# Kernel tuning notes

Measured on AMD Instinct MI355X. Metric: run time of the kernel, lower is better.

## Reference

```python
import jax, jax.numpy as jnp
import numpy as np
from jax import lax

B, D_MODEL, T = 4, 256, 8192
D_STATE, D_CONV = 16, 4
D_INNER = 2 * D_MODEL          # expand=2.0
DT_RANK = (D_MODEL + 15) // 16 # ceil(d_model/16) = 16
EPS = 1e-5


def setup_inputs() -> dict:
    key = jax.random.key(0)
    ks = jax.random.split(key, 12)
    s = lambda k, shape, scale=0.02: (jax.random.normal(k, shape, jnp.float32) * scale)
    x = jax.random.normal(ks[0], (B, D_MODEL, T), jnp.float32)
    ln_w = jnp.ones((D_MODEL,), jnp.float32)
    ln_b = jnp.zeros((D_MODEL,), jnp.float32)
    in_proj_w = s(ks[1], (2 * D_INNER, D_MODEL))
    conv_w = s(ks[2], (D_INNER, 1, D_CONV), 0.1)
    conv_b = jnp.zeros((D_INNER,), jnp.float32)
    x_proj_w = s(ks[3], (DT_RANK + 2 * D_STATE, D_INNER))
    dt_proj_w = s(ks[4], (D_INNER, DT_RANK), 0.1)
    # bias init so softplus(dt_bias) ~ small positive dt, like mamba_ssm
    dt_proj_b = jnp.log(jnp.expm1(jax.random.uniform(ks[5], (D_INNER,), jnp.float32, 0.001, 0.1)))
    # S4D-real init: A_log = log(1..d_state) broadcast over d_inner
    A_log = jnp.log(jnp.tile(jnp.arange(1, D_STATE + 1, dtype=jnp.float32), (D_INNER, 1)))
    D = jnp.ones((D_INNER,), jnp.float32)
    out_proj_w = s(ks[6], (D_MODEL, D_INNER))
    return {"x": x, "ln_w": ln_w, "ln_b": ln_b, "in_proj_w": in_proj_w,
            "conv_w": conv_w, "conv_b": conv_b, "x_proj_w": x_proj_w,
            "dt_proj_w": dt_proj_w, "dt_proj_b": dt_proj_b, "A_log": A_log,
            "D": D, "out_proj_w": out_proj_w}


def _mamba_block(x, ln_w, ln_b, in_proj_w, conv_w, conv_b, x_proj_w,
                 dt_proj_w, dt_proj_b, A_log, D, out_proj_w):
    # x: (B, C, T)
    residual = x
    xt = jnp.transpose(x, (0, 2, 1))  # (B, T, C)
    # channel layernorm
    mu = jnp.mean(xt, axis=-1, keepdims=True)
    var = jnp.var(xt, axis=-1, keepdims=True)
    xn = (xt - mu) * lax.rsqrt(var + EPS) * ln_w + ln_b
    # in_proj -> x, z
    xz = jnp.einsum('btc,ec->bte', xn, in_proj_w)  # (B,T,2*d_inner)
    x_in, z = jnp.split(xz, 2, axis=-1)
    # causal depthwise conv over time
    xc = jnp.transpose(x_in, (0, 2, 1))  # (B, d_inner, T)
    xc = lax.conv_general_dilated(xc, conv_w, window_strides=(1,),
                                  padding=[(D_CONV - 1, 0)],
                                  dimension_numbers=('NCH', 'OIH', 'NCH'),
                                  feature_group_count=D_INNER)
    xc = xc + conv_b[None, :, None]
    u = jax.nn.silu(jnp.transpose(xc, (0, 2, 1)))  # (B,T,d_inner)
    # x_proj -> dt, B, C
    dbl = jnp.einsum('btd,ed->bte', u, x_proj_w)
    dt, Bm, Cm = jnp.split(dbl, [DT_RANK, DT_RANK + D_STATE], axis=-1)
    delta = jax.nn.softplus(jnp.einsum('btr,dr->btd', dt, dt_proj_w) + dt_proj_b)  # (B,T,d_inner)
    A = -jnp.exp(A_log)  # (d_inner, d_state)
    deltaA = jnp.exp(jnp.einsum('btd,dn->btdn', delta, A))          # (B,T,d,n)
    deltaBu = jnp.einsum('btd,btn->btdn', delta * u, Bm)            # (B,T,d,n)
    # selective scan over time
    def step(h, inp):
        dA_t, dBu_t, C_t = inp
        h = dA_t * h + dBu_t                       # (B,d,n)
        y = jnp.einsum('bdn,bn->bd', h, C_t)
        return h, y
    h0 = jnp.zeros((x.shape[0], D_INNER, D_STATE), x.dtype)
    _, ys = lax.scan(step, h0, (jnp.moveaxis(deltaA, 1, 0),
                                jnp.moveaxis(deltaBu, 1, 0),
                                jnp.moveaxis(Cm, 1, 0)))
    y = jnp.moveaxis(ys, 0, 1) + u * D             # (B,T,d_inner)
    y = y * jax.nn.silu(z)
    out = jnp.einsum('btd,cd->btc', y, out_proj_w)  # (B,T,C)
    return jnp.transpose(out, (0, 2, 1)) + residual


def reference(x, ln_w, ln_b, in_proj_w, conv_w, conv_b, x_proj_w,
              dt_proj_w, dt_proj_b, A_log, D, out_proj_w):
    return _mamba_block(x, ln_w, ln_b, in_proj_w, conv_w, conv_b, x_proj_w,
                        dt_proj_w, dt_proj_b, A_log, D, out_proj_w)
```

## Files before the change

kernel.cpp:

```cpp
#include <hip/hip_runtime.h>

typedef unsigned short u16;
typedef unsigned int u32;
typedef __bf16 bfx8 __attribute__((ext_vector_type(8)));
typedef float f32x4 __attribute__((ext_vector_type(4)));

#define Tn 8192
#define Bn 4
#define MTOT 32768
#define CH 128
#define TC 64

#define OFF_W     0ul
#define OFF_AL2   917504ul
#define OFF_XN    (1ul<<20)
#define OFF_XIN   (17ul<<20)
#define OFF_Z     (49ul<<20)
#define OFF_U     (81ul<<20)
#define OFF_DBLDT (113ul<<20)
#define OFF_BCF   (115ul<<20)
#define OFF_DELTA (119ul<<20)
#define OFF_P     (151ul<<20)
#define OFF_CC    (167ul<<20)

__device__ __forceinline__ float b2f(u16 h){ return __uint_as_float(((u32)h)<<16); }
__device__ __forceinline__ u16 f2b(float f){
  u32 u = __float_as_uint(f);
  return (u16)((u + 0x7FFFu + ((u>>16)&1u)) >> 16);
}
__device__ __forceinline__ float aexp2(float x){ float r; asm("v_exp_f32 %0, %1" : "=v"(r) : "v"(x)); return r; }
__device__ __forceinline__ float arcp (float x){ float r; asm("v_rcp_f32 %0, %1" : "=v"(r) : "v"(x)); return r; }
__device__ __forceinline__ float alog2(float x){ float r; asm("v_log_f32 %0, %1" : "=v"(r) : "v"(x)); return r; }
__device__ __forceinline__ float fsilu(float a){ return a*arcp(1.f + aexp2(-a*1.44269504f)); }
__device__ __forceinline__ float fsoftplus(float v){
  float r = 0.69314718f*alog2(1.f + aexp2(v*1.44269504f));
  return (v > 20.f) ? v : r;
}
typedef const __attribute__((address_space(1))) void* gp1_t;
typedef __attribute__((address_space(3))) void* lp3_t;
__device__ __forceinline__ void gload_lds16(const void* g, void* l){
  __builtin_amdgcn_global_load_lds((gp1_t)g, (lp3_t)l, 16, 0, 0);
}

__global__ void wconv_k(const float* __restrict__ inw, const float* __restrict__ xpw,
                        const float* __restrict__ dtw, const float* __restrict__ opw,
                        const float* __restrict__ alog, u16* __restrict__ W, float* __restrict__ aL2)
{
  int i = blockIdx.x*256 + threadIdx.x;
  if (i < 262144) { W[i] = f2b(inw[i]); return; }
  if (i < 294912) { int j = i - 262144; int r = j >> 9, k = j & 511;
    float v = (r < 16) ? xpw[r*512 + k] : ((r < 32) ? 0.f : xpw[(r-16)*512 + k]);
    W[i] = f2b(v); return; }
  if (i < 311296) { int j = i - 294912; int d = j >> 5, k = j & 31;
    W[i] = f2b((k < 16) ? dtw[d*16 + k] : 0.f); return; }
  if (i < 442368) { W[i] = f2b(opw[i - 311296]); return; }
  if (i < 450560) { int j = i - 442368; aL2[j] = -__expf(alog[j]) * 1.44269504088896f; return; }
}

__global__ __launch_bounds__(256)
void ln_k(const float* __restrict__ x, const float* __restrict__ lnw,
          const float* __restrict__ lnb, u16* __restrict__ xn)
{
  const int t0 = blockIdx.x*64, b = blockIdx.y;
  const int tid = threadIdx.x, cg = tid>>6, tl = tid&63;
  __shared__ float ps[4][64], pq[4][64], mu[64], rs[64];
  float s = 0.f, q = 0.f;
  for (int ci = 0; ci < 64; ci++){
    int c = ci*4 + cg;
    float v = x[((size_t)(b*256 + c))*Tn + t0 + tl];
    s += v; q += v*v;
  }
  ps[cg][tl] = s; pq[cg][tl] = q;
  __syncthreads();
  if (tid < 64){
    float S = ps[0][tid]+ps[1][tid]+ps[2][tid]+ps[3][tid];
    float Q = pq[0][tid]+pq[1][tid]+pq[2][tid]+pq[3][tid];
    float m = S*(1.f/256.f);
    float var = Q*(1.f/256.f) - m*m;
    mu[tid] = m; rs[tid] = rsqrtf(var + 1e-5f);
  }
  __syncthreads();
  const float w = lnw[tid&255], bb = lnb[tid&255];
  for (int t = 0; t < 64; t++){
    float v = x[((size_t)(b*256 + tid))*Tn + t0 + t];
    xn[((size_t)(b*Tn) + t0 + t)*256 + tid] = f2b((v - mu[t])*rs[t]*w + bb);
  }
}

template<int BN, int EPI>
__global__ __launch_bounds__(256)
void gemm_k(const u16* __restrict__ A, int lda,
            const u16* __restrict__ Bw, int ldb,
            u16* __restrict__ O, u16* __restrict__ O2, float* __restrict__ Of, int ldo,
            const float* __restrict__ bias, int K)
{
  constexpr int NFR = BN/32;
  __shared__ __align__(16) u16 sA[128*32];
  __shared__ __align__(16) u16 sB[BN*32];
  const int tid = threadIdx.x;
  const int m0 = blockIdx.x*128, n0 = blockIdx.y*BN;
  const int lane = tid & 63, wid = tid >> 6;
  const int wr = wid >> 1, wc = wid & 1;
  const int lr = lane & 15, g = lane >> 4;
  const f32x4 fz = {0.f,0.f,0.f,0.f};
  f32x4 acc[4][NFR];
  #pragma unroll
  for (int m=0;m<4;m++)
    #pragma unroll
    for (int n=0;n<NFR;n++) acc[m][n] = fz;
  const int nk = K >> 5;
  for (int kt = 0; kt < nk; ++kt){
    __syncthreads();
    #pragma unroll
    for (int i=0;i<2;i++){ int ci = i*256 + tid;
      gload_lds16(A + (size_t)(m0+(ci>>2))*lda + kt*32 + (ci&3)*8, sA + ci*8); }
    #pragma unroll
    for (int i=0;i<BN/64;i++){ int ci = i*256 + tid;
      gload_lds16(Bw + (size_t)(n0+(ci>>2))*ldb + kt*32 + (ci&3)*8, sB + ci*8); }
    __syncthreads();
    bfx8 af[4], bf[NFR];
    #pragma unroll
    for (int m=0;m<4;m++) af[m] = *(const bfx8*)(sA + (wr*64 + m*16 + lr)*32 + g*8);
    #pragma unroll
    for (int n=0;n<NFR;n++) bf[n] = *(const bfx8*)(sB + (wc*(BN/2) + n*16 + lr)*32 + g*8);
    #pragma unroll
    for (int m=0;m<4;m++)
      #pragma unroll
      for (int n=0;n<NFR;n++)
        acc[m][n] = __builtin_amdgcn_mfma_f32_16x16x32_bf16(af[m], bf[n], acc[m][n], 0, 0, 0);
  }
  #pragma unroll
  for (int m=0;m<4;m++)
    #pragma unroll
    for (int n=0;n<NFR;n++)
      #pragma unroll
      for (int r=0;r<4;r++){
        int row = m0 + wr*64 + m*16 + g*4 + r;
        int col = n0 + wc*(BN/2) + n*16 + lr;
        float v = acc[m][n][r];
        if (EPI == 0){
          O[(size_t)row*ldo + col] = f2b(v);
        } else if (EPI == 1){
          O[(size_t)row*ldo + col] = f2b(fsoftplus(v + bias[col]));
        } else if (EPI == 2){
          if (col < 512) O[(size_t)row*512 + col] = f2b(v);
          else           O2[(size_t)row*512 + (col-512)] = f2b(v);
        } else {
          if (col < 32) O[(size_t)row*32 + col] = f2b(v);
          else          Of[(size_t)row*32 + (col-32)] = v;
        }
      }
}

__global__ __launch_bounds__(256)
void conv_k(const u16* __restrict__ xin, const float* __restrict__ cw,
            const float* __restrict__ cb, u16* __restrict__ u)
{
  const int t0 = blockIdx.x*32, d0 = blockIdx.y*64, b = blockIdx.z;
  const int tid = threadIdx.x;
  __shared__ float sx[35][64];
  __shared__ float sw[4][64];
  { int d = tid>>2, j = tid&3; sw[j][d] = cw[(d0+d)*4 + j]; }
  for (int i=0;i<9;i++){ int f = i*256 + tid; if (f < 35*64){
      int r = f>>6, dd = f&63; int t = t0 - 3 + r;
      sx[r][dd] = (t >= 0) ? b2f(xin[((size_t)(b*Tn)+t)*512 + d0+dd]) : 0.f; } }
  __syncthreads();
  const float cbv = cb[d0 + (tid&63)];
  for (int oi=0; oi<8; oi++){
    int f = oi*256 + tid; int tr = f>>6, dd = f&63;
    float a = cbv;
    #pragma unroll
    for (int j=0;j<4;j++) a += sw[j][dd]*sx[tr+j][dd];
    u[((size_t)(b*Tn)+t0+tr)*512 + d0+dd] = f2b(fsilu(a));
  }
}

__global__ __launch_bounds__(256)
void scanA_k(const u16* __restrict__ delta, const u16* __restrict__ u,
             const float* __restrict__ bcf, const float* __restrict__ aL2,
             float* __restrict__ P, float* __restrict__ CC)
{
  const int ch = blockIdx.x, d = blockIdx.y*256 + threadIdx.x, b = blockIdx.z;
  const int t0 = ch*TC;
  float aL[16], h[16];
  #pragma unroll
  for (int i=0;i<4;i++) *(f32x4*)(aL+4*i) = *(const f32x4*)(aL2 + (size_t)d*16 + 4*i);
  #pragma unroll
  for (int n=0;n<16;n++) h[n] = 0.f;
  bool st = true;
  #pragma unroll
  for (int n=1;n<16;n++) st = st && (fabsf(aL[n] - (n+1)*aL[0]) <= 2e-4f*fabsf(aL[n]));
  const u16* dp = delta + (size_t)(b*Tn + t0)*512 + d;
  const u16* up = u     + (size_t)(b*Tn + t0)*512 + d;
  const float* bp = bcf + (size_t)(b*Tn + t0)*32;
  float sdlt = 0.f;
  const float aL0 = aL[0];
  if (st){
    for (int t=0;t<TC;t++){
      float dlt = b2f(dp[(size_t)t*512]);
      float uu  = b2f(up[(size_t)t*512]);
      float Bv[16];
      #pragma unroll
      for (int i=0;i<4;i++) *(f32x4*)(Bv+4*i) = *(const f32x4*)(bp + (size_t)t*32 + 4*i);
      float du = dlt*uu; sdlt += dlt;
      float r = aexp2(dlt*aL0);
      float r2 = r*r, e = r, f = r2;
      #pragma unroll
      for (int n=0;n<16;n+=2){
        h[n]   = fmaf(e, h[n],   du*Bv[n]);
        h[n+1] = fmaf(f, h[n+1], du*Bv[n+1]);
        e *= r2; f *= r2;
      }
    }
  } else {
    for (int t=0;t<TC;t++){
      float dlt = b2f(dp[(size_t)t*512]);
      float uu  = b2f(up[(size_t)t*512]);
      float Bv[16];
      #pragma unroll
      for (int i=0;i<4;i++) *(f32x4*)(Bv+4*i) = *(const f32x4*)(bp + (size_t)t*32 + 4*i);
      float du = dlt*uu; sdlt += dlt;
      #pragma unroll
      for (int n=0;n<16;n++)
        h[n] = fmaf(aexp2(dlt*aL[n]), h[n], du*Bv[n]);
    }
  }
  float Pq[16];
  #pragma unroll
  for (int n=0;n<16;n++) Pq[n] = aexp2(sdlt*aL[n]);
  size_t o = ((size_t)((b*CH+ch)*512 + d))<<4;
  #pragma unroll
  for (int i=0;i<4;i++){
    *(f32x4*)(P +o+4*i) = *(f32x4*)(Pq+4*i);
    *(f32x4*)(CC+o+4*i) = *(f32x4*)(h +4*i);
  }
}

__global__ __launch_bounds__(256)
void scanB_k(float* __restrict__ P, const float* __restrict__ CC)
{
  const int gid = blockIdx.x*256 + threadIdx.x;
  const int b = gid >> 11, r = gid & 2047;
  const size_t base = (size_t)(r>>2)*16 + (size_t)(r&3)*4;
  f32x4 h = {0.f,0.f,0.f,0.f};
  #pragma unroll 4
  for (int ch=0; ch<CH; ch++){
    size_t idx = ((size_t)(b*CH+ch))*8192 + base;
    f32x4 Pv = *(f32x4*)(P+idx);
    f32x4 cv = *(const f32x4*)(CC+idx);
    *(f32x4*)(P+idx) = h;
    h = Pv*h + cv;
  }
}

__global__ __launch_bounds__(256)
void scanC_k(const u16* __restrict__ delta, const u16* __restrict__ u,
             const float* __restrict__ bcf, const u16* __restrict__ z,
             const float* __restrict__ aL2, const float* __restrict__ h0,
             const float* __restrict__ Dp, u16* __restrict__ yg)
{
  const int ch = blockIdx.x, d = blockIdx.y*256 + threadIdx.x, b = blockIdx.z;
  const int t0 = ch*TC;
  float aL[16], h[16];
  #pragma unroll
  for (int i=0;i<4;i++) *(f32x4*)(aL+4*i) = *(const f32x4*)(aL2 + (size_t)d*16 + 4*i);
  size_t o = ((size_t)((b*CH+ch)*512 + d))<<4;
  #pragma unroll
  for (int i=0;i<4;i++) *(f32x4*)(h+4*i) = *(const f32x4*)(h0+o+4*i);
  bool st = true;
  #pragma unroll
  for (int n=1;n<16;n++) st = st && (fabsf(aL[n] - (n+1)*aL[0]) <= 2e-4f*fabsf(aL[n]));
  const float Dd = Dp[d];
  const float aL0 = aL[0];
  const u16* dp = delta + (size_t)(b*Tn + t0)*512 + d;
  const u16* up = u     + (size_t)(b*Tn + t0)*512 + d;
  const u16* zp = z     + (size_t)(b*Tn + t0)*512 + d;
  const float* bp = bcf + (size_t)(b*Tn + t0)*32;
  u16* yp = yg + (size_t)(b*Tn + t0)*512 + d;
  if (st){
    for (int t=0;t<TC;t++){
      float dlt = b2f(dp[(size_t)t*512]);
      float uu  = b2f(up[(size_t)t*512]);
      float zz  = b2f(zp[(size_t)t*512]);
      float Bv[16], Cv[16];
      #pragma unroll
      for (int i=0;i<4;i++){
        *(f32x4*)(Bv+4*i) = *(const f32x4*)(bp + (size_t)t*32 + 4*i);
        *(f32x4*)(Cv+4*i) = *(const f32x4*)(bp + (size_t)t*32 + 16 + 4*i);
      }
      float du = dlt*uu;
      float r = aexp2(dlt*aL0);
      float r2 = r*r, e = r, f = r2;
      float p0=0.f, p1=0.f;
      #pragma unroll
      for (int n=0;n<16;n+=2){
        h[n]   = fmaf(e, h[n],   du*Bv[n]);   p0 = fmaf(h[n],   Cv[n],   p0);
        h[n+1] = fmaf(f, h[n+1], du*Bv[n+1]); p1 = fmaf(h[n+1], Cv[n+1], p1);
        e *= r2; f *= r2;
      }
      float p = p0 + p1;
      float gy = (p + uu*Dd) * fsilu(zz);
      yp[(size_t)t*512] = f2b(gy);
    }
  } else {
    for (int t=0;t<TC;t++){
      float dlt = b2f(dp[(size_t)t*512]);
      float uu  = b2f(up[(size_t)t*512]);
      float zz  = b2f(zp[(size_t)t*512]);
      float Bv[16], Cv[16];
      #pragma unroll
      for (int i=0;i<4;i++){
        *(f32x4*)(Bv+4*i) = *(const f32x4*)(bp + (size_t)t*32 + 4*i);
        *(f32x4*)(Cv+4*i) = *(const f32x4*)(bp + (size_t)t*32 + 16 + 4*i);
      }
      float du = dlt*uu;
      float p0 = 0.f;
      #pragma unroll
      for (int n=0;n<16;n++){
        h[n] = fmaf(aexp2(dlt*aL[n]), h[n], du*Bv[n]);
        p0 = fmaf(h[n], Cv[n], p0);
      }
      float gy = (p0 + uu*Dd) * fsilu(zz);
      yp[(size_t)t*512] = f2b(gy);
    }
  }
}

__global__ __launch_bounds__(256)
void transres_k(const u16* __restrict__ yt, const float* __restrict__ x, float* __restrict__ out)
{
  const int t0 = blockIdx.x*64, c0 = blockIdx.y*64, b = blockIdx.z;
  const int tid = threadIdx.x;
  __shared__ float st[64][65];
  for (int i=0;i<16;i++){ int f=i*256+tid; int tr=f>>6, cc=f&63;
    st[tr][cc] = b2f(yt[((size_t)(b*Tn)+t0+tr)*256 + c0+cc]); }
  __syncthreads();
  for (int i=0;i<16;i++){ int f=i*256+tid; int cr=f>>6, tt=f&63;
    size_t oa = ((size_t)(b*256)+c0+cr)*Tn + t0+tt;
    out[oa] = st[tt][cr] + x[oa]; }
}

extern "C" void kernel_launch(void* const* d_in, const int* in_sizes, int n_in,
                              void* d_out, int out_size, void* d_ws, size_t ws_size,
                              hipStream_t stream)
{
  const float* x    = (const float*)d_in[0];
  const float* lnw  = (const float*)d_in[1];
  const float* lnb  = (const float*)d_in[2];
  const float* inw  = (const float*)d_in[3];
  const float* cw   = (const float*)d_in[4];
  const float* cb   = (const float*)d_in[5];
  const float* xpw  = (const float*)d_in[6];
  const float* dtw  = (const float*)d_in[7];
  const float* dtb  = (const float*)d_in[8];
  const float* alog = (const float*)d_in[9];
  const float* Dp   = (const float*)d_in[10];
  const float* opw  = (const float*)d_in[11];
  float* out = (float*)d_out;
  char* ws = (char*)d_ws;

  u16*   W     = (u16*)(ws + OFF_W);
  float* aL2   = (float*)(ws + OFF_AL2);
  u16*   xn    = (u16*)(ws + OFF_XN);
  u16*   xin   = (u16*)(ws + OFF_XIN);
  u16*   z     = (u16*)(ws + OFF_Z);
  u16*   u     = (u16*)(ws + OFF_U);
  u16*   dblDT = (u16*)(ws + OFF_DBLDT);
  float* bcf   = (float*)(ws + OFF_BCF);
  u16*   delta = (u16*)(ws + OFF_DELTA);
  float* P     = (float*)(ws + OFF_P);
  float* CC    = (float*)(ws + OFF_CC);
  u16*   yg    = xin;
  u16*   ytmp  = xn;

  wconv_k<<<1760, 256, 0, stream>>>(inw, xpw, dtw, opw, alog, W, aL2);
  ln_k<<<dim3(Tn/64, Bn), 256, 0, stream>>>(x, lnw, lnb, xn);
  gemm_k<128,2><<<dim3(MTOT/128, 8), 256, 0, stream>>>(xn, 256, W, 256, xin, z, nullptr, 512, nullptr, 256);
  conv_k<<<dim3(Tn/32, 8, Bn), 256, 0, stream>>>(xin, cw, cb, u);
  gemm_k<64,3><<<dim3(MTOT/128, 1), 256, 0, stream>>>(u, 512, W + 262144, 512, dblDT, nullptr, bcf, 32, nullptr, 512);
  gemm_k<128,1><<<dim3(MTOT/128, 4), 256, 0, stream>>>(dblDT, 32, W + 294912, 32, delta, nullptr, nullptr, 512, dtb, 32);
  scanA_k<<<dim3(CH, 2, Bn), 256, 0, stream>>>(delta, u, bcf, aL2, P, CC);
  scanB_k<<<32, 256, 0, stream>>>(P, CC);
  scanC_k<<<dim3(CH, 2, Bn), 256, 0, stream>>>(delta, u, bcf, z, aL2, P, Dp, yg);
  gemm_k<128,0><<<dim3(MTOT/128, 2), 256, 0, stream>>>(yg, 512, W + 311296, 512, ytmp, nullptr, nullptr, 256, nullptr, 512);
  transres_k<<<dim3(Tn/64, 4, Bn), 256, 0, stream>>>(ytmp, x, out);
}
```

Measured before the change: 230.3 us.

## Fuse dt_proj+softplus into scan kernels and out_proj with transpose-residual

Removes the separate dt_proj GEMM and its bf16 delta buffer. Each scan kernel now recomputes delta per timestep from the 16-wide fp32 dt-rank projection, using a dot product with dt_proj weights followed by softplus. The output projection GEMM is fused with the transpose and residual add through an LDS staging tile, which drops the transres kernel and its intermediate buffer. The scan inner loops use packed fp32 FMA/mul instructions, and scanB is changed to scalar per-thread work across more blocks. The trade is extra ALU work in both scan passes in exchange for less memory traffic and fewer launches.

```diff
diff --git a/kernel.cpp b/kernel.cpp
--- a/kernel.cpp
+++ b/kernel.cpp
@@ -4,6 +4,7 @@
 typedef unsigned int u32;
 typedef __bf16 bfx8 __attribute__((ext_vector_type(8)));
 typedef float f32x4 __attribute__((ext_vector_type(4)));
+typedef float f32x2 __attribute__((ext_vector_type(2)));
 
 #define Tn 8192
 #define Bn 4
@@ -17,11 +18,10 @@
 #define OFF_XIN   (17ul<<20)
 #define OFF_Z     (49ul<<20)
 #define OFF_U     (81ul<<20)
-#define OFF_DBLDT (113ul<<20)
+#define OFF_DTF   (113ul<<20)
 #define OFF_BCF   (115ul<<20)
-#define OFF_DELTA (119ul<<20)
-#define OFF_P     (151ul<<20)
-#define OFF_CC    (167ul<<20)
+#define OFF_P     (119ul<<20)
+#define OFF_CC    (136ul<<20)
 
 __device__ __forceinline__ float b2f(u16 h){ return __uint_as_float(((u32)h)<<16); }
 __device__ __forceinline__ u16 f2b(float f){
@@ -36,6 +36,12 @@
   float r = 0.69314718f*alog2(1.f + aexp2(v*1.44269504f));
   return (v > 20.f) ? v : r;
 }
+__device__ __forceinline__ f32x2 pk_fma(f32x2 a, f32x2 b, f32x2 c){
+  f32x2 d; asm("v_pk_fma_f32 %0, %1, %2, %3" : "=v"(d) : "v"(a), "v"(b), "v"(c)); return d;
+}
+__device__ __forceinline__ f32x2 pk_mul(f32x2 a, f32x2 b){
+  f32x2 d; asm("v_pk_mul_f32 %0, %1, %2" : "=v"(d) : "v"(a), "v"(b)); return d;
+}
 typedef const __attribute__((address_space(1))) void* gp1_t;
 typedef __attribute__((address_space(3))) void* lp3_t;
 __device__ __forceinline__ void gload_lds16(const void* g, void* l){
@@ -43,7 +49,7 @@
 }
 
 __global__ void wconv_k(const float* __restrict__ inw, const float* __restrict__ xpw,
-                        const float* __restrict__ dtw, const float* __restrict__ opw,
+                        const float* __restrict__ opw,
                         const float* __restrict__ alog, u16* __restrict__ W, float* __restrict__ aL2)
 {
   int i = blockIdx.x*256 + threadIdx.x;
@@ -51,10 +57,8 @@
   if (i < 294912) { int j = i - 262144; int r = j >> 9, k = j & 511;
     float v = (r < 16) ? xpw[r*512 + k] : ((r < 32) ? 0.f : xpw[(r-16)*512 + k]);
     W[i] = f2b(v); return; }
-  if (i < 311296) { int j = i - 294912; int d = j >> 5, k = j & 31;
-    W[i] = f2b((k < 16) ? dtw[d*16 + k] : 0.f); return; }
-  if (i < 442368) { W[i] = f2b(opw[i - 311296]); return; }
-  if (i < 450560) { int j = i - 442368; aL2[j] = -__expf(alog[j]) * 1.44269504088896f; return; }
+  if (i < 425984) { W[i + 16384] = f2b(opw[i - 294912]); return; }
+  if (i < 434176) { int j = i - 425984; aL2[j] = -__expf(alog[j]) * 1.44269504088896f; return; }
 }
 
 __global__ __launch_bounds__(256)
@@ -91,8 +95,8 @@
 __global__ __launch_bounds__(256)
 void gemm_k(const u16* __restrict__ A, int lda,
             const u16* __restrict__ Bw, int ldb,
-            u16* __restrict__ O, u16* __restrict__ O2, float* __restrict__ Of, int ldo,
-            const float* __restrict__ bias, int K)
+            u16* __restrict__ O, u16* __restrict__ O2, float* __restrict__ Of,
+            float* __restrict__ Of2, int ldo, int K)
 {
   constexpr int NFR = BN/32;
   __shared__ __align__(16) u16 sA[128*32];
@@ -138,18 +142,76 @@
         int row = m0 + wr*64 + m*16 + g*4 + r;
         int col = n0 + wc*(BN/2) + n*16 + lr;
         float v = acc[m][n][r];
-        if (EPI == 0){
-          O[(size_t)row*ldo + col] = f2b(v);
-        } else if (EPI == 1){
-          O[(size_t)row*ldo + col] = f2b(fsoftplus(v + bias[col]));
-        } else if (EPI == 2){
+        if (EPI == 2){
           if (col < 512) O[(size_t)row*512 + col] = f2b(v);
           else           O2[(size_t)row*512 + (col-512)] = f2b(v);
         } else {
-          if (col < 32) O[(size_t)row*32 + col] = f2b(v);
-          else          Of[(size_t)row*32 + (col-32)] = v;
+          if (col < 16)       Of [(size_t)row*16 + col] = v;
+          else if (col >= 32) Of2[(size_t)row*32 + (col-32)] = v;
         }
       }
+}
+
+__global__ __launch_bounds__(256)
+void gemmot_k(const u16* __restrict__ A, const u16* __restrict__ Bw,
+              const float* __restrict__ x, float* __restrict__ out)
+{
+  __shared__ __align__(16) u16 sA[128*32];
+  __shared__ __align__(16) u16 sB[128*32];
+  __shared__ float st[64][129];
+  const int tid = threadIdx.x;
+  const int m0 = blockIdx.x*128, n0 = blockIdx.y*128;
+  const int lane = tid & 63, wid = tid >> 6;
+  const int wr = wid >> 1, wc = wid & 1;
+  const int lr = lane & 15, g = lane >> 4;
+  const f32x4 fz = {0.f,0.f,0.f,0.f};
+  f32x4 acc[4][4];
+  #pragma unroll
+  for (int m=0;m<4;m++)
+    #pragma unroll
+    for (int n=0;n<4;n++) acc[m][n] = fz;
+  for (int kt = 0; kt < 16; ++kt){
+    __syncthreads();
+    #pragma unroll
+    for (int i=0;i<2;i++){ int ci = i*256 + tid;
+      gload_lds16(A + (size_t)(m0+(ci>>2))*512 + kt*32 + (ci&3)*8, sA + ci*8); }
+    #pragma unroll
+    for (int i=0;i<2;i++){ int ci = i*256 + tid;
+      gload_lds16(Bw + (size_t)(n0+(ci>>2))*512 + kt*32 + (ci&3)*8, sB + ci*8); }
+    __syncthreads();
+    bfx8 af[4], bf[4];
+    #pragma unroll
+    for (int m=0;m<4;m++) af[m] = *(const bfx8*)(sA + (wr*64 + m*16 + lr)*32 + g*8);
+    #pragma unroll
+    for (int n=0;n<4;n++) bf[n] = *(const bfx8*)(sB + (wc*64 + n*16 + lr)*32 + g*8);
+    #pragma unroll
+    for (int m=0;m<4;m++)
+      #pragma unroll
+      for (int n=0;n<4;n++)
+        acc[m][n] = __builtin_amdgcn_mfma_f32_16x16x32_bf16(af[m], bf[n], acc[m][n], 0, 0, 0);
+  }
+  const int b = m0 >> 13, t0 = m0 & 8191;
+  const int tl = tid & 63, cgrp = tid >> 6;
+  for (int hf=0; hf<2; hf++){
+    __syncthreads();
+    if (wr == hf){
+      #pragma unroll
+      for (int m=0;m<4;m++)
+        #pragma unroll
+        for (int n=0;n<4;n++)
+          #pragma unroll
+          for (int r=0;r<4;r++)
+            st[m*16 + g*4 + r][wc*64 + n*16 + lr] = acc[m][n][r];
+    }
+    __syncthreads();
+    const int tg = t0 + hf*64 + tl;
+    #pragma unroll
+    for (int ci=0; ci<32; ci++){
+      int c = cgrp*32 + ci;
+      size_t oa = ((size_t)(b*256) + n0 + c)*Tn + tg;
+      out[oa] = st[tl][c] + x[oa];
+    }
+  }
 }
 
 __global__ __launch_bounds__(256)
@@ -176,49 +238,69 @@
 }
 
 __global__ __launch_bounds__(256)
-void scanA_k(const u16* __restrict__ delta, const u16* __restrict__ u,
-             const float* __restrict__ bcf, const float* __restrict__ aL2,
+void scanA_k(const float* __restrict__ dtf, const float* __restrict__ dtw, const float* __restrict__ dtb,
+             const u16* __restrict__ u, const float* __restrict__ bcf, const float* __restrict__ aL2,
              float* __restrict__ P, float* __restrict__ CC)
 {
   const int ch = blockIdx.x, d = blockIdx.y*256 + threadIdx.x, b = blockIdx.z;
   const int t0 = ch*TC;
-  float aL[16], h[16];
-  #pragma unroll
-  for (int i=0;i<4;i++) *(f32x4*)(aL+4*i) = *(const f32x4*)(aL2 + (size_t)d*16 + 4*i);
-  #pragma unroll
-  for (int n=0;n<16;n++) h[n] = 0.f;
+  float h[16], wv[16];
+  #pragma unroll
+  for (int i=0;i<4;i++) *(f32x4*)(wv+4*i) = *(const f32x4*)(dtw + (size_t)d*16 + 4*i);
+  #pragma unroll
+  for (int n=0;n<16;n++) h[n]=0.f;
+  const float dtbd = dtb[d];
+  const float aL0 = aL2[(size_t)d*16];
   bool st = true;
   #pragma unroll
-  for (int n=1;n<16;n++) st = st && (fabsf(aL[n] - (n+1)*aL[0]) <= 2e-4f*fabsf(aL[n]));
-  const u16* dp = delta + (size_t)(b*Tn + t0)*512 + d;
-  const u16* up = u     + (size_t)(b*Tn + t0)*512 + d;
+  for (int i=0;i<4;i++){
+    f32x4 av = *(const f32x4*)(aL2 + (size_t)d*16 + 4*i);
+    #pragma unroll
+    for (int k=0;k<4;k++){ int n = 4*i+k; st = st && (fabsf(av[k]-(n+1)*aL0) <= 2e-4f*fabsf(av[k])); }
+  }
+  const float* dtp = dtf + (size_t)(b*Tn + t0)*16;
+  const u16* up = u + (size_t)(b*Tn + t0)*512 + d;
   const float* bp = bcf + (size_t)(b*Tn + t0)*32;
   float sdlt = 0.f;
-  const float aL0 = aL[0];
   if (st){
     for (int t=0;t<TC;t++){
-      float dlt = b2f(dp[(size_t)t*512]);
-      float uu  = b2f(up[(size_t)t*512]);
-      float Bv[16];
+      float dr[16], Bv[16];
+      #pragma unroll
+      for (int i=0;i<4;i++) *(f32x4*)(dr+4*i) = *(const f32x4*)(dtp + (size_t)t*16 + 4*i);
       #pragma unroll
       for (int i=0;i<4;i++) *(f32x4*)(Bv+4*i) = *(const f32x4*)(bp + (size_t)t*32 + 4*i);
+      f32x2 a2 = {0.f,0.f};
+      #pragma unroll
+      for (int j=0;j<8;j++) a2 = pk_fma(*(f32x2*)(wv+2*j), *(f32x2*)(dr+2*j), a2);
+      float dlt = fsoftplus(a2.x + a2.y + dtbd);
+      float uu = b2f(up[(size_t)t*512]);
       float du = dlt*uu; sdlt += dlt;
       float r = aexp2(dlt*aL0);
-      float r2 = r*r, e = r, f = r2;
-      #pragma unroll
-      for (int n=0;n<16;n+=2){
-        h[n]   = fmaf(e, h[n],   du*Bv[n]);
-        h[n+1] = fmaf(f, h[n+1], du*Bv[n+1]);
-        e *= r2; f *= r2;
+      float r2 = r*r;
+      f32x2 ef = {r, r2}; const f32x2 rr = {r2, r2}; const f32x2 du2 = {du, du};
+      #pragma unroll
+      for (int j=0;j<8;j++){
+        f32x2 hb = *(f32x2*)(h+2*j);
+        hb = pk_fma(ef, hb, pk_mul(du2, *(f32x2*)(Bv+2*j)));
+        *(f32x2*)(h+2*j) = hb;
+        ef = pk_mul(ef, rr);
       }
     }
   } else {
+    float aL[16];
+    #pragma unroll
+    for (int i=0;i<4;i++) *(f32x4*)(aL+4*i) = *(const f32x4*)(aL2 + (size_t)d*16 + 4*i);
     for (int t=0;t<TC;t++){
-      float dlt = b2f(dp[(size_t)t*512]);
-      float uu  = b2f(up[(size_t)t*512]);
-      float Bv[16];
+      float dr[16], Bv[16];
+      #pragma unroll
+      for (int i=0;i<4;i++) *(f32x4*)(dr+4*i) = *(const f32x4*)(dtp + (size_t)t*16 + 4*i);
       #pragma unroll
       for (int i=0;i<4;i++) *(f32x4*)(Bv+4*i) = *(const f32x4*)(bp + (size_t)t*32 + 4*i);
+      float dot = dtbd;
+      #pragma unroll
+      for (int k=0;k<16;k++) dot = fmaf(wv[k], dr[k], dot);
+      float dlt = fsoftplus(dot);
+      float uu = b2f(up[(size_t)t*512]);
       float du = dlt*uu; sdlt += dlt;
       #pragma unroll
       for (int n=0;n<16;n++)
@@ -227,7 +309,11 @@
   }
   float Pq[16];
   #pragma unroll
-  for (int n=0;n<16;n++) Pq[n] = aexp2(sdlt*aL[n]);
+  for (int i=0;i<4;i++){
+    f32x4 av = *(const f32x4*)(aL2 + (size_t)d*16 + 4*i);
+    #pragma unroll
+    for (int k=0;k<4;k++) Pq[4*i+k] = aexp2(sdlt*av[k]);
+  }
   size_t o = ((size_t)((b*CH+ch)*512 + d))<<4;
   #pragma unroll
   for (int i=0;i<4;i++){
@@ -240,79 +326,100 @@
 void scanB_k(float* __restrict__ P, const float* __restrict__ CC)
 {
   const int gid = blockIdx.x*256 + threadIdx.x;
-  const int b = gid >> 11, r = gid & 2047;
-  const size_t base = (size_t)(r>>2)*16 + (size_t)(r&3)*4;
-  f32x4 h = {0.f,0.f,0.f,0.f};
+  const int b = gid >> 13, r = gid & 8191;
+  const size_t base = (size_t)b*CH*8192 + r;
+  float h = 0.f;
   #pragma unroll 4
   for (int ch=0; ch<CH; ch++){
-    size_t idx = ((size_t)(b*CH+ch))*8192 + base;
-    f32x4 Pv = *(f32x4*)(P+idx);
-    f32x4 cv = *(const f32x4*)(CC+idx);
-    *(f32x4*)(P+idx) = h;
-    h = Pv*h + cv;
-  }
-}
-
-__global__ __launch_bounds__(256)
-void scanC_k(const u16* __restrict__ delta, const u16* __restrict__ u,
-             const float* __restrict__ bcf, const u16* __restrict__ z,
+    size_t idx = base + (size_t)ch*8192;
+    float Pv = P[idx];
+    float cv = CC[idx];
+    P[idx] = h;
+    h = fmaf(Pv, h, cv);
+  }
+}
+
+__global__ __launch_bounds__(256)
+void scanC_k(const float* __restrict__ dtf, const float* __restrict__ dtw, const float* __restrict__ dtb,
+             const u16* __restrict__ u, const float* __restrict__ bcf, const u16* __restrict__ z,
              const float* __restrict__ aL2, const float* __restrict__ h0,
              const float* __restrict__ Dp, u16* __restrict__ yg)
 {
   const int ch = blockIdx.x, d = blockIdx.y*256 + threadIdx.x, b = blockIdx.z;
   const int t0 = ch*TC;
-  float aL[16], h[16];
-  #pragma unroll
-  for (int i=0;i<4;i++) *(f32x4*)(aL+4*i) = *(const f32x4*)(aL2 + (size_t)d*16 + 4*i);
+  float h[16], wv[16];
+  #pragma unroll
+  for (int i=0;i<4;i++) *(f32x4*)(wv+4*i) = *(const f32x4*)(dtw + (size_t)d*16 + 4*i);
   size_t o = ((size_t)((b*CH+ch)*512 + d))<<4;
   #pragma unroll
   for (int i=0;i<4;i++) *(f32x4*)(h+4*i) = *(const f32x4*)(h0+o+4*i);
+  const float dtbd = dtb[d];
+  const float Dd = Dp[d];
+  const float aL0 = aL2[(size_t)d*16];
   bool st = true;
   #pragma unroll
-  for (int n=1;n<16;n++) st = st && (fabsf(aL[n] - (n+1)*aL[0]) <= 2e-4f*fabsf(aL[n]));
-  const float Dd = Dp[d];
-  const float aL0 = aL[0];
-  const u16* dp = delta + (size_t)(b*Tn + t0)*512 + d;
-  const u16* up = u     + (size_t)(b*Tn + t0)*512 + d;
-  const u16* zp = z     + (size_t)(b*Tn + t0)*512 + d;
+  for (int i=0;i<4;i++){
+    f32x4 av = *(const f32x4*)(aL2 + (size_t)d*16 + 4*i);
+    #pragma unroll
+    for (int k=0;k<4;k++){ int n = 4*i+k; st = st && (fabsf(av[k]-(n+1)*aL0) <= 2e-4f*fabsf(av[k])); }
+  }
+  const float* dtp = dtf + (size_t)(b*Tn + t0)*16;
+  const u16* up = u + (size_t)(b*Tn + t0)*512 + d;
+  const u16* zp = z + (size_t)(b*Tn + t0)*512 + d;
   const float* bp = bcf + (size_t)(b*Tn + t0)*32;
   u16* yp = yg + (size_t)(b*Tn + t0)*512 + d;
   if (st){
     for (int t=0;t<TC;t++){
-      float dlt = b2f(dp[(size_t)t*512]);
-      float uu  = b2f(up[(size_t)t*512]);
-      float zz  = b2f(zp[(size_t)t*512]);
-      float Bv[16], Cv[16];
+      float dr[16], Bv[16], Cv[16];
+      #pragma unroll
+      for (int i=0;i<4;i++) *(f32x4*)(dr+4*i) = *(const f32x4*)(dtp + (size_t)t*16 + 4*i);
       #pragma unroll
       for (int i=0;i<4;i++){
         *(f32x4*)(Bv+4*i) = *(const f32x4*)(bp + (size_t)t*32 + 4*i);
         *(f32x4*)(Cv+4*i) = *(const f32x4*)(bp + (size_t)t*32 + 16 + 4*i);
       }
+      f32x2 a2 = {0.f,0.f};
+      #pragma unroll
+      for (int j=0;j<8;j++) a2 = pk_fma(*(f32x2*)(wv+2*j), *(f32x2*)(dr+2*j), a2);
+      float dlt = fsoftplus(a2.x + a2.y + dtbd);
+      float uu = b2f(up[(size_t)t*512]);
+      float zz = b2f(zp[(size_t)t*512]);
       float du = dlt*uu;
       float r = aexp2(dlt*aL0);
-      float r2 = r*r, e = r, f = r2;
-      float p0=0.f, p1=0.f;
-      #pragma unroll
-      for (int n=0;n<16;n+=2){
-        h[n]   = fmaf(e, h[n],   du*Bv[n]);   p0 = fmaf(h[n],   Cv[n],   p0);
-        h[n+1] = fmaf(f, h[n+1], du*Bv[n+1]); p1 = fmaf(h[n+1], Cv[n+1], p1);
-        e *= r2; f *= r2;
-      }
-      float p = p0 + p1;
+      float r2 = r*r;
+      f32x2 ef = {r, r2}; const f32x2 rr = {r2, r2}; const f32x2 du2 = {du, du};
+      f32x2 p2 = {0.f,0.f};
+      #pragma unroll
+      for (int j=0;j<8;j++){
+        f32x2 hb = *(f32x2*)(h+2*j);
+        hb = pk_fma(ef, hb, pk_mul(du2, *(f32x2*)(Bv+2*j)));
+        *(f32x2*)(h+2*j) = hb;
+        p2 = pk_fma(hb, *(f32x2*)(Cv+2*j), p2);
+        ef = pk_mul(ef, rr);
+      }
+      float p = p2.x + p2.y;
       float gy = (p + uu*Dd) * fsilu(zz);
       yp[(size_t)t*512] = f2b(gy);
     }
   } else {
+    float aL[16];
+    #pragma unroll
+    for (int i=0;i<4;i++) *(f32x4*)(aL+4*i) = *(const f32x4*)(aL2 + (size_t)d*16 + 4*i);
     for (int t=0;t<TC;t++){
-      float dlt = b2f(dp[(size_t)t*512]);
-      float uu  = b2f(up[(size_t)t*512]);
-      float zz  = b2f(zp[(size_t)t*512]);
-      float Bv[16], Cv[16];
+      float dr[16], Bv[16], Cv[16];
+      #pragma unroll
+      for (int i=0;i<4;i++) *(f32x4*)(dr+4*i) = *(const f32x4*)(dtp + (size_t)t*16 + 4*i);
       #pragma unroll
       for (int i=0;i<4;i++){
         *(f32x4*)(Bv+4*i) = *(const f32x4*)(bp + (size_t)t*32 + 4*i);
         *(f32x4*)(Cv+4*i) = *(const f32x4*)(bp + (size_t)t*32 + 16 + 4*i);
       }
+      float dot = dtbd;
+      #pragma unroll
+      for (int k=0;k<16;k++) dot = fmaf(wv[k], dr[k], dot);
+      float dlt = fsoftplus(dot);
+      float uu = b2f(up[(size_t)t*512]);
+      float zz = b2f(zp[(size_t)t*512]);
       float du = dlt*uu;
       float p0 = 0.f;
       #pragma unroll
@@ -324,20 +431,6 @@
       yp[(size_t)t*512] = f2b(gy);
     }
   }
-}
-
-__global__ __launch_bounds__(256)
-void transres_k(const u16* __restrict__ yt, const float* __restrict__ x, float* __restrict__ out)
-{
-  const int t0 = blockIdx.x*64, c0 = blockIdx.y*64, b = blockIdx.z;
-  const int tid = threadIdx.x;
-  __shared__ float st[64][65];
-  for (int i=0;i<16;i++){ int f=i*256+tid; int tr=f>>6, cc=f&63;
-    st[tr][cc] = b2f(yt[((size_t)(b*Tn)+t0+tr)*256 + c0+cc]); }
-  __syncthreads();
-  for (int i=0;i<16;i++){ int f=i*256+tid; int cr=f>>6, tt=f&63;
-    size_t oa = ((size_t)(b*256)+c0+cr)*Tn + t0+tt;
-    out[oa] = st[tt][cr] + x[oa]; }
 }
 
 extern "C" void kernel_launch(void* const* d_in, const int* in_sizes, int n_in,
@@ -365,23 +458,19 @@
   u16*   xin   = (u16*)(ws + OFF_XIN);
   u16*   z     = (u16*)(ws + OFF_Z);
   u16*   u     = (u16*)(ws + OFF_U);
-  u16*   dblDT = (u16*)(ws + OFF_DBLDT);
+  float* dtf   = (float*)(ws + OFF_DTF);
   float* bcf   = (float*)(ws + OFF_BCF);
-  u16*   delta = (u16*)(ws + OFF_DELTA);
   float* P     = (float*)(ws + OFF_P);
   float* CC    = (float*)(ws + OFF_CC);
   u16*   yg    = xin;
-  u16*   ytmp  = xn;
-
-  wconv_k<<<1760, 256, 0, stream>>>(inw, xpw, dtw, opw, alog, W, aL2);
+
+  wconv_k<<<1696, 256, 0, stream>>>(inw, xpw, opw, alog, W, aL2);
   ln_k<<<dim3(Tn/64, Bn), 256, 0, stream>>>(x, lnw, lnb, xn);
-  gemm_k<128,2><<<dim3(MTOT/128, 8), 256, 0, stream>>>(xn, 256, W, 256, xin, z, nullptr, 512, nullptr, 256);
+  gemm_k<128,2><<<dim3(MTOT/128, 8), 256, 0, stream>>>(xn, 256, W, 256, xin, z, nullptr, nullptr, 512, 256);
   conv_k<<<dim3(Tn/32, 8, Bn), 256, 0, stream>>>(xin, cw, cb, u);
-  gemm_k<64,3><<<dim3(MTOT/128, 1), 256, 0, stream>>>(u, 512, W + 262144, 512, dblDT, nullptr, bcf, 32, nullptr, 512);
-  gemm_k<128,1><<<dim3(MTOT/128, 4), 256, 0, stream>>>(dblDT, 32, W + 294912, 32, delta, nullptr, nullptr, 512, dtb, 32);
-  scanA_k<<<dim3(CH, 2, Bn), 256, 0, stream>>>(delta, u, bcf, aL2, P, CC);
-  scanB_k<<<32, 256, 0, stream>>>(P, CC);
-  scanC_k<<<dim3(CH, 2, Bn), 256, 0, stream>>>(delta, u, bcf, z, aL2, P, Dp, yg);
-  gemm_k<128,0><<<dim3(MTOT/128, 2), 256, 0, stream>>>(yg, 512, W + 311296, 512, ytmp, nullptr, nullptr, 256, nullptr, 512);
-  transres_k<<<dim3(Tn/64, 4, Bn), 256, 0, stream>>>(ytmp, x, out);
-}
+  gemm_k<64,3><<<dim3(MTOT/128, 1), 256, 0, stream>>>(u, 512, W + 262144, 512, nullptr, nullptr, dtf, bcf, 0, 512);
+  scanA_k<<<dim3(CH, 2, Bn), 256, 0, stream>>>(dtf, dtw, dtb, u, bcf, aL2, P, CC);
+  scanB_k<<<128, 256, 0, stream>>>(P, CC);
+  scanC_k<<<dim3(CH, 2, Bn), 256, 0, stream>>>(dtf, dtw, dtb, u, bcf, z, aL2, P, Dp, yg);
+  gemmot_k<<<dim3(MTOT/128, 2), 256, 0, stream>>>(yg, W + 311296, x, out);
+}
```

Result: slower. 272.7 us (+18.4%).
